# Kernel tuning notes

Measured on AMD Instinct MI355X. Metric: run time of the kernel, lower is better.

## Reference

```python
import jax, jax.numpy as jnp
import numpy as np

N_FILTER = 128
IMAGE_SIZE = 64
CHANNELS = 3
LAT_SIZE = 512
N_CALLS = 2 * 16  # n_calls * 16 sequential CA steps
EPS = 1e-5       # InstanceNorm2d default eps

_SOBEL_X = np.array([[-1.0, 0.0, 1.0], [-2.0, 0.0, 2.0], [-1.0, 0.0, 1.0]], np.float32) / 8.0
_SOBEL_Y = _SOBEL_X.T.copy()
_SOBEL_K = jnp.asarray(np.stack([_SOBEL_X, _SOBEL_Y])[:, None])  # [2,1,3,3]


def sobel_perception(x):
    # x: [B,C,H,W] -> [B,3C,H,W] = concat(identity, grad_x, grad_y)
    B, C, H, W = x.shape
    g = jax.lax.conv_general_dilated(
        x.reshape(B * C, 1, H, W), _SOBEL_K, (1, 1), 'SAME',
        dimension_numbers=('NCHW', 'OIHW', 'NCHW'))
    g = g.reshape(B, C, 2, H, W)
    return jnp.concatenate([x, g[:, :, 0], g[:, :, 1]], axis=1)


def instance_norm(x):
    # per (b, c) normalization over H, W (affine=False)
    m = jnp.mean(x, axis=(2, 3), keepdims=True)
    v = jnp.var(x, axis=(2, 3), keepdims=True)
    return (x - m) * jax.lax.rsqrt(v + EPS)


def setup_inputs() -> dict:
    key = jax.random.key(0)
    k1, k2, k3 = jax.random.split(key, 3)
    C = N_FILTER
    n_params = 3 * C * C + C  # dyn conv weight + bias
    return {
        'lat': jax.random.normal(k1, (8, LAT_SIZE), jnp.float32),
        'leak_factor': jnp.ones((), jnp.float32) * 0.1,
        'w_dyn': jax.random.normal(k2, (LAT_SIZE, n_params), jnp.float32) * 0.02,
        'b_dyn': jax.random.normal(k3, (n_params,), jnp.float32) * 0.02,
    }


def reference(lat, leak_factor, w_dyn, b_dyn):
    B = lat.shape[0]
    C, H, W = N_FILTER, IMAGE_SIZE, IMAGE_SIZE
    # ca_seed: zeros with the center cell set to 1 (Growing-NCA style seed)
    seed = jnp.zeros((B, C, H, W), lat.dtype).at[:, :, H // 2, W // 2].set(1.0)

    # latent-conditioned dynamic 1x1 conv params (per sample)
    params = lat @ w_dyn + b_dyn                     # [B, 3C*C + C]
    w = params[:, :3 * C * C].reshape(B, C, 3 * C)   # [B, out, in]
    b = params[:, 3 * C * C:]                        # [B, C]

    lf = jnp.clip(leak_factor, 0.001, 1000.0)

    def step(out, _):
        y = sobel_perception(out)                    # [B,3C,H,W]
        y = instance_norm(y)
        y = jnp.einsum('bihw,boi->bohw', y, w) + b[:, :, None, None]
        out = out + lf * y
        return out, out

    out, embs = jax.lax.scan(step, seed, None, length=N_CALLS)
    out_embs = jnp.concatenate([seed[None], embs], axis=0)  # [N_CALLS+1,B,C,H,W]
    out_raw = out[:, :CHANNELS]
    return jnp.clip(out_raw, -1.0, 1.0), out_embs, out_raw
```

## Files before the change

### kernel.cpp

```cpp
#include <hip/hip_runtime.h>

typedef unsigned short u16;
typedef short short8 __attribute__((ext_vector_type(8)));
typedef float floatx4 __attribute__((ext_vector_type(4)));

#define NB 8
#define NC 128
#define K3 384
#define YC 256
#define HW 4096
#define LATN 512
#define NPAR 49280
#define W2OFF 49152
#define NSTEP 32

#define EMB_OFF 98304
#define EMB_SLICE 4194304
#define RAW_OFF 138510336

__device__ __forceinline__ float bf2f(u16 h) {
    return __uint_as_float(((unsigned)h) << 16);
}
__device__ __forceinline__ u16 f2bf(float f) {
    unsigned u = __float_as_uint(f);
    u += 0x7fffu + ((u >> 16) & 1u);
    return (u16)(u >> 16);
}
__device__ __forceinline__ void splitbf(float f, u16& hi, u16& lo) {
    unsigned u = __float_as_uint(f);
    hi = (u16)(u >> 16);
    lo = f2bf(f - __uint_as_float(u & 0xFFFF0000u));
}

__global__ void k_detect(const unsigned* __restrict__ lfp,
                         int* __restrict__ flag, float* __restrict__ lfF) {
    unsigned bits = lfp[0];
    int isf32 = ((bits & 0xFFFFu) == 0xCCCDu);
    float lf = isf32 ? __uint_as_float(bits) : bf2f((u16)(bits & 0xFFFFu));
    flag[0] = isf32;
    lfF[0] = fminf(fmaxf(lf, 0.001f), 1000.0f);
}

__global__ __launch_bounds__(256) void k_init(const void* __restrict__ lat,
                                              const int* __restrict__ flag,
                                              float* __restrict__ latF,
                                              float* __restrict__ state,
                                              void* __restrict__ outv) {
    int isf32 = flag[0];
    int e = blockIdx.x * 256 + threadIdx.x;
    if (e < NB * LATN)
        latF[e] = isf32 ? ((const float*)lat)[e] : bf2f(((const u16*)lat)[e]);
    float v = ((e & (HW - 1)) == 2080) ? 1.0f : 0.0f;
    state[e] = v;
    if (isf32) ((float*)outv)[EMB_OFF + e] = v;
    else       ((u16*)outv)[EMB_OFF + e] = f2bf(v);
}

__global__ __launch_bounds__(256) void k_params(const float* __restrict__ latF,
                                                const void* __restrict__ w_dyn,
                                                const void* __restrict__ b_dyn,
                                                const int* __restrict__ flag,
                                                u16* __restrict__ Wh,
                                                u16* __restrict__ Wl,
                                                float* __restrict__ biasP) {
    int isf32 = flag[0];
    int j = blockIdx.x * 256 + threadIdx.x;
    if (j >= NPAR) return;
    float acc[NB] = {};
    if (isf32) {
        const float* wd = (const float*)w_dyn;
        for (int k = 0; k < LATN; k++) {
            float wv = wd[(size_t)k * NPAR + j];
#pragma unroll
            for (int b = 0; b < NB; b++) acc[b] += latF[b * LATN + k] * wv;
        }
    } else {
        const u16* wd = (const u16*)w_dyn;
        for (int k = 0; k < LATN; k++) {
            float wv = bf2f(wd[(size_t)k * NPAR + j]);
#pragma unroll
            for (int b = 0; b < NB; b++) acc[b] += latF[b * LATN + k] * wv;
        }
    }
    float bd = isf32 ? ((const float*)b_dyn)[j] : bf2f(((const u16*)b_dyn)[j]);
    if (j < W2OFF) {
#pragma unroll
        for (int b = 0; b < NB; b++) {
            u16 hi, lo;
            splitbf(acc[b] + bd, hi, lo);
            Wh[(size_t)b * W2OFF + j] = hi;
            Wl[(size_t)b * W2OFF + j] = lo;
        }
    } else {
#pragma unroll
        for (int b = 0; b < NB; b++) biasP[b * NC + (j - W2OFF)] = acc[b] + bd;
    }
}

__global__ __launch_bounds__(256) void k_sobel(const float* __restrict__ state,
                                               u16* __restrict__ Yh,
                                               u16* __restrict__ Yl,
                                               float* __restrict__ statM,
                                               float* __restrict__ statR) {
    int blk = blockIdx.x;
    int b = blk & 7, c = blk >> 3;
    const float* xp = state + ((size_t)(b * NC + c)) * HW;
    __shared__ float smf[66 * 68];
    __shared__ float red[4][3];
    __shared__ float bc[6];
    int tid = threadIdx.x;
    int lane = tid & 63, w = tid >> 6;
    if (tid < 68) smf[tid] = 0.f;
    else if (tid < 136) smf[65 * 68 + (tid - 68)] = 0.f;
    else if (tid < 200) smf[(tid - 135) * 68 + 64] = 0.f;
    float4 ld[4];
#pragma unroll
    for (int q = 0; q < 4; q++)
        ld[q] = *(const float4*)(xp + q * 1024 + tid * 4);
#pragma unroll
    for (int q = 0; q < 4; q++) {
        int idx = q * 1024 + tid * 4;
        *(float4*)&smf[((idx >> 6) + 1) * 68 + (idx & 63)] = ld[q];
    }
    __syncthreads();
    int rr = tid >> 2, c0 = (tid & 3) << 4;
    const float* r0 = smf + rr * 68 + c0;
    const float* r1 = r0 + 68;
    const float* r2 = r1 + 68;
    float xv[16], gxv[16], gyv[16];
    float a00, a10, a20;
    if (c0 == 0) { a00 = 0.f; a10 = 0.f; a20 = 0.f; }
    else { a00 = r0[-1]; a10 = r1[-1]; a20 = r2[-1]; }
    float a01 = r0[0], a11 = r1[0], a21 = r2[0];
    float sx = 0, sgx = 0, sgy = 0;
#pragma unroll
    for (int u = 0; u < 16; u++) {
        float a02 = r0[u + 1], a12 = r1[u + 1], a22 = r2[u + 1];
        float x  = a11;
        float gx = (a02 - a00 + 2.f * (a12 - a10) + a22 - a20) * 0.125f;
        float gy = (a20 + 2.f * a21 + a22 - a00 - 2.f * a01 - a02) * 0.125f;
        xv[u] = x; gxv[u] = gx; gyv[u] = gy;
        sx += x; sgx += gx; sgy += gy;
        a00 = a01; a01 = a02; a10 = a11; a11 = a12; a20 = a21; a21 = a22;
    }
#pragma unroll
    for (int off = 32; off >= 1; off >>= 1) {
        sx += __shfl_down(sx, off); sgx += __shfl_down(sgx, off); sgy += __shfl_down(sgy, off);
    }
    if (lane == 0) { red[w][0] = sx; red[w][1] = sgx; red[w][2] = sgy; }
    __syncthreads();
    if (tid == 0) {
        float t0 = 0, t1 = 0, t2 = 0;
        for (int i = 0; i < 4; i++) { t0 += red[i][0]; t1 += red[i][1]; t2 += red[i][2]; }
        float m0 = t0 * (1.f / HW);
        bc[0] = m0; bc[1] = t1 * (1.f / HW); bc[2] = t2 * (1.f / HW);
        statM[b * 128 + c] = m0;
    }
    __syncthreads();
    float mx = bc[0], mgx = bc[1], mgy = bc[2];
    float vx = 0, vgx = 0, vgy = 0;
#pragma unroll
    for (int u = 0; u < 16; u++) {
        float dx = xv[u] - mx, dgx = gxv[u] - mgx, dgy = gyv[u] - mgy;
        vx += dx * dx; vgx += dgx * dgx; vgy += dgy * dgy;
    }
#pragma unroll
    for (int off = 32; off >= 1; off >>= 1) {
        vx += __shfl_down(vx, off); vgx += __shfl_down(vgx, off); vgy += __shfl_down(vgy, off);
    }
    __syncthreads();
    if (lane == 0) { red[w][0] = vx; red[w][1] = vgx; red[w][2] = vgy; }
    __syncthreads();
    if (tid == 0) {
        float t0 = 0, t1 = 0, t2 = 0;
        for (int i = 0; i < 4; i++) { t0 += red[i][0]; t1 += red[i][1]; t2 += red[i][2]; }
        float r0v = rsqrtf(t0 * (1.f / HW) + 1e-5f);
        bc[3] = r0v;
        bc[4] = rsqrtf(t1 * (1.f / HW) + 1e-5f);
        bc[5] = rsqrtf(t2 * (1.f / HW) + 1e-5f);
        statR[b * 128 + c] = r0v;
    }
    __syncthreads();
    float rgx = bc[4], rgy = bc[5];

    int ph[2][8], pl[2][8];
#pragma unroll
    for (int u = 0; u < 16; u++) {
        float yv[2] = { (gxv[u] - mgx) * rgx, (gyv[u] - mgy) * rgy };
#pragma unroll
        for (int t = 0; t < 2; t++) {
            u16 hi, lo;
            splitbf(yv[t], hi, lo);
            if ((u & 1) == 0) { ph[t][u >> 1] = hi; pl[t][u >> 1] = lo; }
            else { ph[t][u >> 1] |= (unsigned)hi << 16; pl[t][u >> 1] |= (unsigned)lo << 16; }
        }
    }
    int p0 = rr * 64 + c0;
#pragma unroll
    for (int t = 0; t < 2; t++) {
        size_t base = (size_t)(b * YC + t * 128 + c) * HW + p0;
        ((int4*)(Yh + base))[0] = make_int4(ph[t][0], ph[t][1], ph[t][2], ph[t][3]);
        ((int4*)(Yh + base))[1] = make_int4(ph[t][4], ph[t][5], ph[t][6], ph[t][7]);
        ((int4*)(Yl + base))[0] = make_int4(pl[t][0], pl[t][1], pl[t][2], pl[t][3]);
        ((int4*)(Yl + base))[1] = make_int4(pl[t][4], pl[t][5], pl[t][6], pl[t][7]);
    }
}

__global__ __launch_bounds__(256, 4) void k_mix(const u16* __restrict__ Yh,
                                                const u16* __restrict__ Yl,
                                                const u16* __restrict__ Wh,
                                                const u16* __restrict__ Wl,
                                                const float* __restrict__ biasP,
                                                const float* __restrict__ statM,
                                                const float* __restrict__ statR,
                                                const float* __restrict__ lfF,
                                                const int* __restrict__ flag,
                                                float* __restrict__ state,
                                                void* __restrict__ outv,
                                                int step) {
    int isf32 = flag[0];
    float lf = lfF[0];
    int b  = blockIdx.x & 7;
    int pt = (blockIdx.x >> 3) << 5;
    int tid = threadIdx.x;
    int lane = tid & 63, w = tid >> 6;
    int lq = lane >> 4, lr = lane & 15;

    __shared__ __align__(16) u16 Bh[2][32 * 34];
    __shared__ __align__(16) u16 Bl[2][32 * 34];
    __shared__ float sM[128], sR[128];
    __shared__ __align__(16) float sX[128 * 36];

    if (tid < 128) sM[tid] = statM[b * 128 + tid];
    else           sR[tid - 128] = statR[b * 128 + tid - 128];

    floatx4 acc[2][2] = {};
    size_t aoff = ((size_t)(b * NC + w * 32 + lr)) * K3 + lq * 8;
    const u16* Ahb = Wh + aoff;
    const u16* Alb = Wl + aoff;

    int xs_c = tid >> 3;
    int xs_p = (tid & 7) << 2;
    int ys_k = (tid & 127) >> 2;
    int ys_p = (tid & 3) << 3;
    int fb   = lq * 8 * 34 + lr;

    const float* xbase = state + (size_t)(b * NC) * HW + pt;
    float4 f0 = *(const float4*)(xbase + (size_t)xs_c * HW + xs_p);
    int4 sv;
    __syncthreads();

    for (int kc = 0; kc < 12; kc++) {
        unsigned* BhW = (unsigned*)Bh[kc & 1];
        unsigned* BlW = (unsigned*)Bl[kc & 1];
        if (kc < 4) {
            int ca = (kc << 5) + xs_c;
            float mA = sM[ca], rA = sR[ca];
            *(float4*)&sX[ca * 36 + xs_p] = f0;
            u16 h0, h1, h2, h3, l0, l1, l2, l3;
            splitbf((f0.x - mA) * rA, h0, l0);
            splitbf((f0.y - mA) * rA, h1, l1);
            splitbf((f0.z - mA) * rA, h2, l2);
            splitbf((f0.w - mA) * rA, h3, l3);
            int dwA = (xs_c * 34 + xs_p) >> 1;
            BhW[dwA]     = (unsigned)h0 | ((unsigned)h1 << 16);
            BhW[dwA + 1] = (unsigned)h2 | ((unsigned)h3 << 16);
            BlW[dwA]     = (unsigned)l0 | ((unsigned)l1 << 16);
            BlW[dwA + 1] = (unsigned)l2 | ((unsigned)l3 << 16);
        } else {
            int dw = (ys_k * 34 + ys_p) >> 1;
            unsigned* BW = (tid < 128) ? BhW : BlW;
            BW[dw]     = sv.x; BW[dw + 1] = sv.y; BW[dw + 2] = sv.z; BW[dw + 3] = sv.w;
        }
        if (kc < 3) {
            const float* sp = xbase + (size_t)((kc + 1) << 5) * HW;
            f0 = *(const float4*)(sp + (size_t)xs_c * HW + xs_p);
        } else if (kc < 11) {
            size_t yb = ((size_t)(b * YC + ((kc - 3) << 5) + ys_k)) * HW + pt + ys_p;
            sv = (tid < 128) ? *(const int4*)(Yh + yb) : *(const int4*)(Yl + yb);
        }
        asm volatile("s_waitcnt lgkmcnt(0)\n\ts_barrier" ::: "memory");

        int k0 = kc << 5;
        short8 ah[2], al[2];
#pragma unroll
        for (int mi = 0; mi < 2; mi++) {
            ah[mi] = *(const short8*)(Ahb + (size_t)mi * 16 * K3 + k0);
            al[mi] = *(const short8*)(Alb + (size_t)mi * 16 * K3 + k0);
        }
        const u16* BhR = Bh[kc & 1];
        const u16* BlR = Bl[kc & 1];
        short8 bh[2], bl[2];
#pragma unroll
        for (int ni = 0; ni < 2; ni++)
#pragma unroll
            for (int j = 0; j < 8; j++) {
                bh[ni][j] = (short)BhR[fb + j * 34 + ni * 16];
                bl[ni][j] = (short)BlR[fb + j * 34 + ni * 16];
            }
#pragma unroll
        for (int mi = 0; mi < 2; mi++)
#pragma unroll
            for (int ni = 0; ni < 2; ni++) {
                acc[mi][ni] = __builtin_amdgcn_mfma_f32_16x16x32_bf16(ah[mi], bh[ni], acc[mi][ni], 0, 0, 0);
                acc[mi][ni] = __builtin_amdgcn_mfma_f32_16x16x32_bf16(al[mi], bh[ni], acc[mi][ni], 0, 0, 0);
                acc[mi][ni] = __builtin_amdgcn_mfma_f32_16x16x32_bf16(ah[mi], bl[ni], acc[mi][ni], 0, 0, 0);
            }
    }

    size_t embb = (size_t)EMB_OFF + (size_t)(step + 1) * EMB_SLICE;
#pragma unroll
    for (int mi = 0; mi < 2; mi++) {
#pragma unroll
        for (int ni = 0; ni < 2; ni++) {
#pragma unroll
            for (int r = 0; r < 4; r++) {
                int o = w * 32 + mi * 16 + lq * 4 + r;
                int pcol = ni * 16 + lr;
                int p = pt + pcol;
                float val = acc[mi][ni][r] + biasP[b * NC + o];
                size_t si = ((size_t)(b * NC + o)) * HW + p;
                float ns = sX[o * 36 + pcol] + lf * val;
                state[si] = ns;
                size_t ei = embb + (size_t)(b * NC + o) * HW + p;
                if (isf32) ((float*)outv)[ei] = ns;
                else       ((u16*)outv)[ei] = f2bf(ns);
                if (step == NSTEP - 1 && o < 3) {
                    int ri = (b * 3 + o) * HW + p;
                    float cl = fminf(fmaxf(ns, -1.f), 1.f);
                    if (isf32) {
                        ((float*)outv)[ri] = cl;
                        ((float*)outv)[(size_t)RAW_OFF + ri] = ns;
                    } else {
                        ((u16*)outv)[ri] = f2bf(cl);
                        ((u16*)outv)[(size_t)RAW_OFF + ri] = f2bf(ns);
                    }
                }
            }
        }
    }
}

extern "C" void kernel_launch(void* const* d_in, const int* in_sizes, int n_in,
                              void* d_out, int out_size, void* d_ws, size_t ws_size,
                              hipStream_t stream) {
    const void* lat   = d_in[0];
    const void* lfp   = d_in[1];
    const void* w_dyn = d_in[2];
    const void* b_dyn = d_in[3];
    char* ws = (char*)d_ws;
    size_t off = 0;
    float* state  = (float*)(ws + off); off += (size_t)NB * NC * HW * 4;
    u16*   Yh     = (u16*)  (ws + off); off += (size_t)NB * YC * HW * 2;
    u16*   Yl     = (u16*)  (ws + off); off += (size_t)NB * YC * HW * 2;
    u16*   Wh     = (u16*)  (ws + off); off += (size_t)NB * W2OFF * 2;
    u16*   Wl     = (u16*)  (ws + off); off += (size_t)NB * W2OFF * 2;
    float* biasP  = (float*)(ws + off); off += (size_t)NB * NC * 4;
    float* latF   = (float*)(ws + off); off += (size_t)NB * LATN * 4;
    float* statM  = (float*)(ws + off); off += (size_t)NB * NC * 4;
    float* statR  = (float*)(ws + off); off += (size_t)NB * NC * 4;
    int*   flag   = (int*)  (ws + off); off += 64;
    float* lfF    = (float*)(ws + off); off += 64;

    k_detect<<<1, 1, 0, stream>>>((const unsigned*)lfp, flag, lfF);
    k_init<<<(NB * NC * HW) / 256, 256, 0, stream>>>(lat, flag, latF, state, d_out);
    k_params<<<(NPAR + 255) / 256, 256, 0, stream>>>(latF, w_dyn, b_dyn, flag, Wh, Wl, biasP);
    for (int step = 0; step < NSTEP; step++) {
        k_sobel<<<NB * NC, 256, 0, stream>>>(state, Yh, Yl, statM, statR);
        k_mix<<<NB * NC, 256, 0, stream>>>(Yh, Yl, Wh, Wl, biasP, statM, statR, lfF, flag, state, d_out, step);
    }
}
```

Measured before the change: 1.981 ms.

## Tile Y buffers per pixel-tile and transpose swizzled LDS B operand for vector reads

The perception kernel now writes Yh/Yl in a tiled layout [b][pixel-tile][channel][32], so each mix block reads one contiguous chunk instead of strided rows. In the mix kernel the shared B tiles are stored transposed (pixel-major) with an XOR swizzle and padded to 36, so each lane loads its 8 bf16 MFMA operands with two 8-byte LDS reads instead of 8 scalar u16 reads. In exchange, the LDS writes become scalar 16-bit stores with swizzled addressing, which may add write-side bank conflicts and instruction count.

```diff
diff --git a/kernel.cpp b/kernel.cpp
--- a/kernel.cpp
+++ b/kernel.cpp
@@ -2,6 +2,7 @@
 
 typedef unsigned short u16;
 typedef short short8 __attribute__((ext_vector_type(8)));
+typedef short short4v __attribute__((ext_vector_type(4)));
 typedef float floatx4 __attribute__((ext_vector_type(4)));
 
 #define NB 8
@@ -196,9 +197,10 @@
         }
     }
     int p0 = rr * 64 + c0;
+    int ptI = p0 >> 5, po = p0 & 31;
 #pragma unroll
     for (int t = 0; t < 2; t++) {
-        size_t base = (size_t)(b * YC + t * 128 + c) * HW + p0;
+        size_t base = ((size_t)((b * 128 + ptI) * 256 + t * 128 + c)) * 32 + po;
         ((int4*)(Yh + base))[0] = make_int4(ph[t][0], ph[t][1], ph[t][2], ph[t][3]);
         ((int4*)(Yh + base))[1] = make_int4(ph[t][4], ph[t][5], ph[t][6], ph[t][7]);
         ((int4*)(Yl + base))[0] = make_int4(pl[t][0], pl[t][1], pl[t][2], pl[t][3]);
@@ -221,13 +223,14 @@
     int isf32 = flag[0];
     float lf = lfF[0];
     int b  = blockIdx.x & 7;
-    int pt = (blockIdx.x >> 3) << 5;
+    int ptIdx = blockIdx.x >> 3;
+    int pt = ptIdx << 5;
     int tid = threadIdx.x;
     int lane = tid & 63, w = tid >> 6;
     int lq = lane >> 4, lr = lane & 15;
 
-    __shared__ __align__(16) u16 Bh[2][32 * 34];
-    __shared__ __align__(16) u16 Bl[2][32 * 34];
+    __shared__ __align__(16) u16 Bh[2][32 * 36];
+    __shared__ __align__(16) u16 Bl[2][32 * 36];
     __shared__ float sM[128], sR[128];
     __shared__ __align__(16) float sX[128 * 36];
 
@@ -243,41 +246,59 @@
     int xs_p = (tid & 7) << 2;
     int ys_k = (tid & 127) >> 2;
     int ys_p = (tid & 3) << 3;
-    int fb   = lq * 8 * 34 + lr;
+
+    int fr[2];
+#pragma unroll
+    for (int ni = 0; ni < 2; ni++) {
+        int pcol = ni * 16 + lr;
+        int col = (lq ^ ((pcol >> 1) & 3)) << 3;
+        fr[ni] = pcol * 36 + col;
+    }
 
     const float* xbase = state + (size_t)(b * NC) * HW + pt;
+    const u16* ybh = Yh + (size_t)(b * 128 + ptIdx) * 256 * 32;
+    const u16* ybl = Yl + (size_t)(b * 128 + ptIdx) * 256 * 32;
     float4 f0 = *(const float4*)(xbase + (size_t)xs_c * HW + xs_p);
     int4 sv;
     __syncthreads();
 
     for (int kc = 0; kc < 12; kc++) {
-        unsigned* BhW = (unsigned*)Bh[kc & 1];
-        unsigned* BlW = (unsigned*)Bl[kc & 1];
+        u16* BhW = Bh[kc & 1];
+        u16* BlW = Bl[kc & 1];
         if (kc < 4) {
             int ca = (kc << 5) + xs_c;
             float mA = sM[ca], rA = sR[ca];
             *(float4*)&sX[ca * 36 + xs_p] = f0;
-            u16 h0, h1, h2, h3, l0, l1, l2, l3;
-            splitbf((f0.x - mA) * rA, h0, l0);
-            splitbf((f0.y - mA) * rA, h1, l1);
-            splitbf((f0.z - mA) * rA, h2, l2);
-            splitbf((f0.w - mA) * rA, h3, l3);
-            int dwA = (xs_c * 34 + xs_p) >> 1;
-            BhW[dwA]     = (unsigned)h0 | ((unsigned)h1 << 16);
-            BhW[dwA + 1] = (unsigned)h2 | ((unsigned)h3 << 16);
-            BlW[dwA]     = (unsigned)l0 | ((unsigned)l1 << 16);
-            BlW[dwA + 1] = (unsigned)l2 | ((unsigned)l3 << 16);
+            float vv[4] = { f0.x, f0.y, f0.z, f0.w };
+#pragma unroll
+            for (int i = 0; i < 4; i++) {
+                u16 hi, lo;
+                splitbf((vv[i] - mA) * rA, hi, lo);
+                int px = xs_p + i;
+                int col = xs_c ^ (((px >> 1) & 3) << 3);
+                BhW[px * 36 + col] = hi;
+                BlW[px * 36 + col] = lo;
+            }
         } else {
-            int dw = (ys_k * 34 + ys_p) >> 1;
-            unsigned* BW = (tid < 128) ? BhW : BlW;
-            BW[dw]     = sv.x; BW[dw + 1] = sv.y; BW[dw + 2] = sv.z; BW[dw + 3] = sv.w;
+            u16* BW = (tid < 128) ? BhW : BlW;
+            unsigned uv[4] = { (unsigned)sv.x, (unsigned)sv.y, (unsigned)sv.z, (unsigned)sv.w };
+#pragma unroll
+            for (int i = 0; i < 4; i++) {
+#pragma unroll
+                for (int e2 = 0; e2 < 2; e2++) {
+                    int px = ys_p + i * 2 + e2;
+                    u16 v = (u16)(uv[i] >> (e2 * 16));
+                    int col = ys_k ^ (((px >> 1) & 3) << 3);
+                    BW[px * 36 + col] = v;
+                }
+            }
         }
         if (kc < 3) {
             const float* sp = xbase + (size_t)((kc + 1) << 5) * HW;
             f0 = *(const float4*)(sp + (size_t)xs_c * HW + xs_p);
         } else if (kc < 11) {
-            size_t yb = ((size_t)(b * YC + ((kc - 3) << 5) + ys_k)) * HW + pt + ys_p;
-            sv = (tid < 128) ? *(const int4*)(Yh + yb) : *(const int4*)(Yl + yb);
+            size_t yb = (size_t)(((kc - 3) << 5) + ys_k) * 32 + ys_p;
+            sv = (tid < 128) ? *(const int4*)(ybh + yb) : *(const int4*)(ybl + yb);
         }
         asm volatile("s_waitcnt lgkmcnt(0)\n\ts_barrier" ::: "memory");
 
@@ -292,12 +313,17 @@
         const u16* BlR = Bl[kc & 1];
         short8 bh[2], bl[2];
 #pragma unroll
-        for (int ni = 0; ni < 2; ni++)
-#pragma unroll
-            for (int j = 0; j < 8; j++) {
-                bh[ni][j] = (short)BhR[fb + j * 34 + ni * 16];
-                bl[ni][j] = (short)BlR[fb + j * 34 + ni * 16];
-            }
+        for (int ni = 0; ni < 2; ni++) {
+            short4v h0 = *(const short4v*)(BhR + fr[ni]);
+            short4v h1 = *(const short4v*)(BhR + fr[ni] + 4);
+            short4v l0 = *(const short4v*)(BlR + fr[ni]);
+            short4v l1 = *(const short4v*)(BlR + fr[ni] + 4);
+#pragma unroll
+            for (int j = 0; j < 4; j++) {
+                bh[ni][j] = h0[j]; bh[ni][4 + j] = h1[j];
+                bl[ni][j] = l0[j]; bl[ni][4 + j] = l1[j];
+            }
+        }
 #pragma unroll
         for (int mi = 0; mi < 2; mi++)
 #pragma unroll
```

New measurement: 2.004 ms. Within noise of the previous version (+1.2%).
